# Performance work log

Measured on AMD Instinct MI355X. Metric: run time of the kernel, lower is better.

The kernel has to match this reference:

```python
import jax, jax.numpy as jnp
import numpy as np

ROI_SIZES = (3, 7, 11)
IMAGE_SIZE = 960.0


def setup_inputs() -> dict:
    key = jax.random.key(0)
    ks = jax.random.split(key, 12)
    B, C, H, W = 1, 64, 120, 120
    N = 4096
    feature_maps = jax.random.normal(ks[0], (B, C, H, W), jnp.float32)
    cx = jax.random.uniform(ks[1], (N,), jnp.float32, 100.0, 860.0)
    cy = jax.random.uniform(ks[2], (N,), jnp.float32, 100.0, 860.0)
    bw = jax.random.uniform(ks[3], (N,), jnp.float32, 20.0, 240.0)
    bh = jax.random.uniform(ks[4], (N,), jnp.float32, 20.0, 240.0)
    boxes = jnp.stack([cx - bw / 2, cy - bh / 2, cx + bw / 2, cy + bh / 2], axis=1)
    s = 0.05
    w1 = jax.random.normal(ks[5], (64, 128), jnp.float32) * s
    b1 = jnp.zeros((128,), jnp.float32)
    w2 = jax.random.normal(ks[6], (128, 64), jnp.float32) * s
    b2 = jnp.zeros((64,), jnp.float32)
    p1 = jax.random.normal(ks[7], (256, 128), jnp.float32) * s
    pb1 = jnp.zeros((128,), jnp.float32)
    p2 = jax.random.normal(ks[8], (128, 64), jnp.float32) * s
    pb2 = jnp.zeros((64,), jnp.float32)
    return dict(feature_maps=feature_maps, boxes=boxes, w1=w1, b1=b1, w2=w2, b2=b2,
                p1=p1, pb1=pb1, p2=p2, pb2=pb2)


def _roi_pool(fm0, boxes_norm, r):
    """affine_grid + bilinear grid_sample (align_corners=False, zeros pad) + global avg pool.
    fm0: [C,H,W], boxes_norm: [N,4] in [-1,1]. Returns [N,C]."""
    C, H, W = fm0.shape
    x1, y1, x2, y2 = boxes_norm[:, 0], boxes_norm[:, 1], boxes_norm[:, 2], boxes_norm[:, 3]
    cx = (x1 + x2) / 2
    cy = (y1 + y2) / 2
    bw = jnp.clip(x2 - x1, 1e-6, None)
    bh = jnp.clip(y2 - y1, 1e-6, None)
    # affine_grid base coords with align_corners=False: (2i+1)/r - 1
    lin = (2.0 * jnp.arange(r, dtype=jnp.float32) + 1.0) / r - 1.0
    gx = cx[:, None, None] + (bw / 2)[:, None, None] * lin[None, None, :]  # [N,r,r]
    gy = cy[:, None, None] + (bh / 2)[:, None, None] * lin[None, :, None]  # [N,r,r]
    # normalized -> pixel coords (align_corners=False)
    ix = ((gx + 1.0) * W - 1.0) / 2.0
    iy = ((gy + 1.0) * H - 1.0) / 2.0
    x0f = jnp.floor(ix)
    y0f = jnp.floor(iy)
    wx1 = ix - x0f
    wy1 = iy - y0f
    x0 = x0f.astype(jnp.int32)
    y0 = y0f.astype(jnp.int32)
    fm_flat = fm0.reshape(C, H * W)

    def corner(xi, yi, wt):
        valid = (xi >= 0) & (xi < W) & (yi >= 0) & (yi < H)
        xi_c = jnp.clip(xi, 0, W - 1)
        yi_c = jnp.clip(yi, 0, H - 1)
        idx = yi_c * W + xi_c  # [N,r,r]
        vals = jnp.take(fm_flat, idx.reshape(-1), axis=1).reshape(C, *idx.shape)  # [C,N,r,r]
        return vals * (wt * valid.astype(wt.dtype))[None]

    out = (corner(x0, y0, (1 - wx1) * (1 - wy1))
           + corner(x0 + 1, y0, wx1 * (1 - wy1))
           + corner(x0, y0 + 1, (1 - wx1) * wy1)
           + corner(x0 + 1, y0 + 1, wx1 * wy1))
    return out.mean(axis=(2, 3)).T  # [N,C]


def _shared_head(x, w1, b1, w2, b2):
    h = jax.nn.relu(x @ w1 + b1)
    return jax.nn.relu(h @ w2 + b2)


def reference(feature_maps, boxes, w1, b1, w2, b2, p1, pb1, p2, pb2):
    B, C, H, W = feature_maps.shape
    N = boxes.shape[0]
    boxes_norm = boxes / IMAGE_SIZE * 2.0 - 1.0
    fm0 = feature_maps[0]
    feats = []
    for r in ROI_SIZES:
        pooled = _roi_pool(fm0, boxes_norm, r)  # [N,C]
        feats.append(_shared_head(pooled, w1, b1, w2, b2))
    # global context: avg-pool full map, expand to N
    g = feature_maps.mean(axis=(2, 3))  # [B,C], B=1
    g = jnp.broadcast_to(g, (N, C))
    feats.append(_shared_head(g, w1, b1, w2, b2))
    concat = jnp.concatenate(feats, axis=1)  # [N, 4*64]
    h = jax.nn.relu(concat @ p1 + pb1)
    return jax.nn.relu(h @ p2 + pb2)
```

## Files before the change

kernel.cpp:

```cpp
#include <hip/hip_runtime.h>
#include <hip/hip_bf16.h>


#define HW 120
#define NPIX (HW * HW)

__global__ __launch_bounds__(256) void k_transpose_mean(
    const float* __restrict__ fm, float* __restrict__ fm_t,
    float* __restrict__ partial)
{
    __shared__ float tile[64][65];
    __shared__ float pr[4][64];
    const int t  = threadIdx.x;
    const int tx = t & 63;
    const int ty = t >> 6;
    const int pix0 = blockIdx.x * 64;

    #pragma unroll
    for (int k = 0; k < 16; ++k) {
        const int c = k * 4 + ty;
        tile[c][tx] = fm[c * NPIX + pix0 + tx];
    }
    __syncthreads();
    #pragma unroll
    for (int k = 0; k < 16; ++k) {
        const int p = k * 4 + ty;
        fm_t[(pix0 + p) * 64 + tx] = tile[tx][p];
    }
    float s = 0.f;
    #pragma unroll
    for (int k = 0; k < 16; ++k) s += tile[tx][ty * 16 + k];
    pr[ty][tx] = s;
    __syncthreads();
    if (t < 64)
        partial[blockIdx.x * 64 + t] = pr[0][t] + pr[1][t] + pr[2][t] + pr[3][t];
}

__global__ __launch_bounds__(256) void k_ghead(
    const float* __restrict__ partial,
    const float* __restrict__ w1, const float* __restrict__ b1,
    const float* __restrict__ w2, const float* __restrict__ b2,
    const float* __restrict__ p1, const float* __restrict__ pb1,
    float* __restrict__ f1pre)
{
    __shared__ float pr[4][64];
    __shared__ float g[64];
    __shared__ float h[128];
    __shared__ float gh[64];
    const int t = threadIdx.x;
    const int c = t & 63, q = t >> 6;
    float s = 0.f;
    for (int b = q; b < 225; b += 4) s += partial[b * 64 + c];
    pr[q][c] = s;
    __syncthreads();
    if (t < 64) g[t] = (pr[0][t] + pr[1][t] + pr[2][t] + pr[3][t]) * (1.f / 14400.f);
    __syncthreads();
    if (t < 128) {
        float a = b1[t];
        #pragma unroll 8
        for (int cc = 0; cc < 64; ++cc) a = fmaf(g[cc], w1[cc * 128 + t], a);
        h[t] = fmaxf(a, 0.f);
    }
    __syncthreads();
    if (t < 64) {
        float a = b2[t];
        #pragma unroll 8
        for (int k = 0; k < 128; ++k) a = fmaf(h[k], w2[k * 64 + t], a);
        gh[t] = fmaxf(a, 0.f);
    }
    __syncthreads();
    if (t < 128) {
        float a = pb1[t];
        #pragma unroll 8
        for (int j = 0; j < 64; ++j) a = fmaf(gh[j], p1[(192 + j) * 128 + t], a);
        f1pre[t] = a;
    }
}

template <int R>
__device__ __forceinline__ float4 gather_seg(
    const char* __restrict__ fb, int pg,
    float cx, float cy, float bw2, float bh2)
{
    constexpr float invR = 1.f / (float)R;
    constexpr float s2   = invR * invR;
    float ax = 0.f, ay = 0.f, az = 0.f, aw = 0.f;
    #pragma unroll 2
    for (int lp = pg; lp < R * R; lp += 4) {
        const int i = lp / R;
        const int j = lp - i * R;
        const float liny = (float)(2 * i + 1) * invR - 1.f;
        const float linx = (float)(2 * j + 1) * invR - 1.f;
        const float gy = cy + bh2 * liny;
        const float gx = cx + bw2 * linx;
        const float iy = ((gy + 1.f) * 120.f - 1.f) * 0.5f;
        const float ix = ((gx + 1.f) * 120.f - 1.f) * 0.5f;
        const float y0f = floorf(iy), x0f = floorf(ix);
        const float wy = iy - y0f,  wx = ix - x0f;
        const int y0 = (int)y0f, x0 = (int)x0f;
        const float vy0 = (y0 >= 0 && y0 < HW)      ? 1.f : 0.f;
        const float vy1 = (y0 >= -1 && y0 < HW - 1) ? 1.f : 0.f;
        const float vx0 = (x0 >= 0 && x0 < HW)      ? 1.f : 0.f;
        const float vx1 = (x0 >= -1 && x0 < HW - 1) ? 1.f : 0.f;
        const int x0c = min(max(x0, 0), HW - 1);
        const int x1c = min(max(x0 + 1, 0), HW - 1);
        const int y0c = min(max(y0, 0), HW - 1);
        const int y1c = min(max(y0 + 1, 0), HW - 1);
        const int o00 = (y0c * HW + x0c) * 256;
        const int o01 = (y0c * HW + x1c) * 256;
        const int o10 = (y1c * HW + x0c) * 256;
        const int o11 = (y1c * HW + x1c) * 256;
        const float w00 = (1.f - wx) * (1.f - wy) * s2 * (vy0 * vx0);
        const float w01 = wx * (1.f - wy) * s2 * (vy0 * vx1);
        const float w10 = (1.f - wx) * wy * s2 * (vy1 * vx0);
        const float w11 = wx * wy * s2 * (vy1 * vx1);
        const float4 v0 = *(const float4*)(fb + o00);
        const float4 v1 = *(const float4*)(fb + o01);
        const float4 v2 = *(const float4*)(fb + o10);
        const float4 v3 = *(const float4*)(fb + o11);
        ax = fmaf(w00, v0.x, ax); ay = fmaf(w00, v0.y, ay);
        az = fmaf(w00, v0.z, az); aw = fmaf(w00, v0.w, aw);
        ax = fmaf(w01, v1.x, ax); ay = fmaf(w01, v1.y, ay);
        az = fmaf(w01, v1.z, az); aw = fmaf(w01, v1.w, aw);
        ax = fmaf(w10, v2.x, ax); ay = fmaf(w10, v2.y, ay);
        az = fmaf(w10, v2.z, az); aw = fmaf(w10, v2.w, aw);
        ax = fmaf(w11, v3.x, ax); ay = fmaf(w11, v3.y, ay);
        az = fmaf(w11, v3.z, az); aw = fmaf(w11, v3.w, aw);
    }
    ax += __shfl_xor(ax, 16, 64); ay += __shfl_xor(ay, 16, 64);
    az += __shfl_xor(az, 16, 64); aw += __shfl_xor(aw, 16, 64);
    ax += __shfl_xor(ax, 32, 64); ay += __shfl_xor(ay, 32, 64);
    az += __shfl_xor(az, 32, 64); aw += __shfl_xor(aw, 32, 64);
    return make_float4(ax, ay, az, aw);
}

__global__ __launch_bounds__(256, 8) void k_fused(
    const float* __restrict__ fm_t, const float* __restrict__ boxes,
    const float* __restrict__ w1, const float* __restrict__ b1,
    const float* __restrict__ w2, const float* __restrict__ b2,
    const float* __restrict__ p1, const float* __restrict__ f1pre,
    const float* __restrict__ p2, const float* __restrict__ pb2,
    float* __restrict__ out, int N)
{
    __shared__ __align__(16) float xbufS[4][192];
    __shared__ __align__(16) float hbufS[4][384];
    __shared__ __align__(16) float cbufS[4][192];
    __shared__ __align__(16) float fbufS[4][128];

    const int t    = threadIdx.x;
    const int lane = t & 63;
    const int wid  = t >> 6;
    const int n    = blockIdx.x * 4 + wid;
    if (n >= N) return;

    float* xbuf = xbufS[wid];
    float* hbuf = hbufS[wid];
    float* cbuf = cbufS[wid];
    float* fbuf = fbufS[wid];

    const float4 bx = reinterpret_cast<const float4*>(boxes)[n];
    const float x1 = bx.x / 960.f * 2.f - 1.f;
    const float y1 = bx.y / 960.f * 2.f - 1.f;
    const float x2 = bx.z / 960.f * 2.f - 1.f;
    const float y2 = bx.w / 960.f * 2.f - 1.f;
    const float cx  = (x1 + x2) * 0.5f;
    const float cy  = (y1 + y2) * 0.5f;
    const float bw2 = fmaxf(x2 - x1, 1e-6f) * 0.5f;
    const float bh2 = fmaxf(y2 - y1, 1e-6f) * 0.5f;

    const int qc = lane & 15;
    const int pg = lane >> 4;
    const char* fb = (const char*)fm_t + qc * 16;

    const float4 r0 = gather_seg<3>(fb, pg, cx, cy, bw2, bh2);
    const float4 r1 = gather_seg<7>(fb, pg, cx, cy, bw2, bh2);
    const float4 r2 = gather_seg<11>(fb, pg, cx, cy, bw2, bh2);
    if (pg == 0) {
        *(float4*)(xbuf +       4 * qc) = r0;
        *(float4*)(xbuf +  64 + 4 * qc) = r1;
        *(float4*)(xbuf + 128 + 4 * qc) = r2;
    }

    float h0l, h0h, h1l, h1h, h2l, h2h;
    {
        const float bl = b1[lane], bh = b1[64 + lane];
        h0l = h1l = h2l = bl; h0h = h1h = h2h = bh;
        #define L1STEP(XA0, XA1, XA2, CC) {                                \
            const float wlo = w1[(CC) * 128 + lane];                       \
            const float whi = w1[(CC) * 128 + 64 + lane];                  \
            h0l = fmaf(XA0, wlo, h0l); h0h = fmaf(XA0, whi, h0h);          \
            h1l = fmaf(XA1, wlo, h1l); h1h = fmaf(XA1, whi, h1h);          \
            h2l = fmaf(XA2, wlo, h2l); h2h = fmaf(XA2, whi, h2h); }
        #pragma unroll 4
        for (int k4 = 0; k4 < 16; ++k4) {
            const float4 xv0 = *(const float4*)(xbuf +       4 * k4);
            const float4 xv1 = *(const float4*)(xbuf +  64 + 4 * k4);
            const float4 xv2 = *(const float4*)(xbuf + 128 + 4 * k4);
            L1STEP(xv0.x, xv1.x, xv2.x, 4 * k4 + 0)
            L1STEP(xv0.y, xv1.y, xv2.y, 4 * k4 + 1)
            L1STEP(xv0.z, xv1.z, xv2.z, 4 * k4 + 2)
            L1STEP(xv0.w, xv1.w, xv2.w, 4 * k4 + 3)
        }
        #undef L1STEP
        h0l = fmaxf(h0l, 0.f); h0h = fmaxf(h0h, 0.f);
        h1l = fmaxf(h1l, 0.f); h1h = fmaxf(h1h, 0.f);
        h2l = fmaxf(h2l, 0.f); h2h = fmaxf(h2h, 0.f);
        hbuf[lane]       = h0l; hbuf[64 + lane]  = h0h;
        hbuf[128 + lane] = h1l; hbuf[192 + lane] = h1h;
        hbuf[256 + lane] = h2l; hbuf[320 + lane] = h2h;
    }

    {
        const float bb = b2[lane];
        float c0 = bb, c1 = bb, c2 = bb;
        #define L2STEP(HA0, HA1, HA2, CC) {                                \
            const float wa = w2[(CC) * 64 + lane];                         \
            c0 = fmaf(HA0, wa, c0);                                        \
            c1 = fmaf(HA1, wa, c1);                                        \
            c2 = fmaf(HA2, wa, c2); }
        #pragma unroll 4
        for (int k4 = 0; k4 < 32; ++k4) {
            const float4 hv0 = *(const float4*)(hbuf +       4 * k4);
            const float4 hv1 = *(const float4*)(hbuf + 128 + 4 * k4);
            const float4 hv2 = *(const float4*)(hbuf + 256 + 4 * k4);
            L2STEP(hv0.x, hv1.x, hv2.x, 4 * k4 + 0)
            L2STEP(hv0.y, hv1.y, hv2.y, 4 * k4 + 1)
            L2STEP(hv0.z, hv1.z, hv2.z, 4 * k4 + 2)
            L2STEP(hv0.w, hv1.w, hv2.w, 4 * k4 + 3)
        }
        #undef L2STEP
        cbuf[lane]       = fmaxf(c0, 0.f);
        cbuf[64 + lane]  = fmaxf(c1, 0.f);
        cbuf[128 + lane] = fmaxf(c2, 0.f);
    }

    {
        float flo = f1pre[lane], fhi = f1pre[64 + lane];
        #define L3STEP(CA, QQ) {                                           \
            const float wlo = p1[(QQ) * 128 + lane];                       \
            const float whi = p1[(QQ) * 128 + 64 + lane];                  \
            flo = fmaf(CA, wlo, flo); fhi = fmaf(CA, whi, fhi); }
        #pragma unroll 4
        for (int q4 = 0; q4 < 48; ++q4) {
            const float4 cv = *(const float4*)(cbuf + 4 * q4);
            L3STEP(cv.x, 4 * q4 + 0)
            L3STEP(cv.y, 4 * q4 + 1)
            L3STEP(cv.z, 4 * q4 + 2)
            L3STEP(cv.w, 4 * q4 + 3)
        }
        #undef L3STEP
        fbuf[lane]      = fmaxf(flo, 0.f);
        fbuf[64 + lane] = fmaxf(fhi, 0.f);
    }

    {
        float o = pb2[lane];
        #define L4STEP(FA, JJ) o = fmaf(FA, p2[(JJ) * 64 + lane], o);
        #pragma unroll 4
        for (int j4 = 0; j4 < 32; ++j4) {
            const float4 fv = *(const float4*)(fbuf + 4 * j4);
            L4STEP(fv.x, 4 * j4 + 0)
            L4STEP(fv.y, 4 * j4 + 1)
            L4STEP(fv.z, 4 * j4 + 2)
            L4STEP(fv.w, 4 * j4 + 3)
        }
        #undef L4STEP
        out[n * 64 + lane] = fmaxf(o, 0.f);
    }
}

extern "C" void kernel_launch(void* const* d_in, const int* in_sizes, int n_in,
                              void* d_out, int out_size, void* d_ws, size_t ws_size,
                              hipStream_t stream)
{
    const float* fm    = (const float*)d_in[0];
    const float* boxes = (const float*)d_in[1];
    const float* w1    = (const float*)d_in[2];
    const float* b1    = (const float*)d_in[3];
    const float* w2    = (const float*)d_in[4];
    const float* b2    = (const float*)d_in[5];
    const float* p1    = (const float*)d_in[6];
    const float* pb1   = (const float*)d_in[7];
    const float* p2    = (const float*)d_in[8];
    const float* pb2   = (const float*)d_in[9];
    float* out = (float*)d_out;

    const int N = in_sizes[1] / 4;

    float* ws      = (float*)d_ws;
    float* fm_t    = ws;
    float* partial = fm_t + 921600;
    float* f1pre   = partial + 14400;

    k_transpose_mean<<<NPIX / 64, 256, 0, stream>>>(fm, fm_t, partial);
    k_ghead<<<1, 256, 0, stream>>>(partial, w1, b1, w2, b2, p1, pb1, f1pre);
    k_fused<<<(N + 3) / 4, 256, 0, stream>>>(fm_t, boxes, w1, b1, w2, b2,
                                             p1, f1pre, p2, pb2, out, N);
}
```

Measured before the change: 157.2 us.

## Split each ROI gather across two waves and share MLP work block-wide

The fused kernel goes from 256 to 512 threads per block. Each box's bilinear gather is now split over two waves, and the partial sums are reduced through shared memory. The MLP layers are redistributed so that all 512 threads cooperate across the block's 4 boxes, with __syncthreads between stages instead of one wave per box doing everything. This aims to raise parallelism and cut per-wave serial work, at the cost of block-wide barriers, more shared memory and a reduction step.

Measured after the change: 157.0 us. No clear change (-0.1%).

```diff
diff --git a/kernel.cpp b/kernel.cpp
--- a/kernel.cpp
+++ b/kernel.cpp
@@ -78,15 +78,15 @@
 }
 
 template <int R>
-__device__ __forceinline__ float4 gather_seg(
-    const char* __restrict__ fb, int pg,
+__device__ __forceinline__ float4 gather8(
+    const char* __restrict__ fb, int g8,
     float cx, float cy, float bw2, float bh2)
 {
     constexpr float invR = 1.f / (float)R;
     constexpr float s2   = invR * invR;
     float ax = 0.f, ay = 0.f, az = 0.f, aw = 0.f;
     #pragma unroll 2
-    for (int lp = pg; lp < R * R; lp += 4) {
+    for (int lp = g8; lp < R * R; lp += 8) {
         const int i = lp / R;
         const int j = lp - i * R;
         const float liny = (float)(2 * i + 1) * invR - 1.f;
@@ -134,7 +134,7 @@
     return make_float4(ax, ay, az, aw);
 }
 
-__global__ __launch_bounds__(256, 8) void k_fused(
+__global__ __launch_bounds__(512, 8) void k_fused(
     const float* __restrict__ fm_t, const float* __restrict__ boxes,
     const float* __restrict__ w1, const float* __restrict__ b1,
     const float* __restrict__ w2, const float* __restrict__ b2,
@@ -142,130 +142,166 @@
     const float* __restrict__ p2, const float* __restrict__ pb2,
     float* __restrict__ out, int N)
 {
-    __shared__ __align__(16) float xbufS[4][192];
-    __shared__ __align__(16) float hbufS[4][384];
-    __shared__ __align__(16) float cbufS[4][192];
-    __shared__ __align__(16) float fbufS[4][128];
+    __shared__ __align__(16) float xpart[4][2][192];
+    __shared__ __align__(16) float xbuf[4][192];
+    __shared__ __align__(16) float hbuf[4][384];
+    __shared__ __align__(16) float cbuf[4][192];
+    __shared__ __align__(16) float fbuf[4][128];
+    __shared__ __align__(16) float opart[2][4][64];
 
     const int t    = threadIdx.x;
     const int lane = t & 63;
-    const int wid  = t >> 6;
-    const int n    = blockIdx.x * 4 + wid;
-    if (n >= N) return;
-
-    float* xbuf = xbufS[wid];
-    float* hbuf = hbufS[wid];
-    float* cbuf = cbufS[wid];
-    float* fbuf = fbufS[wid];
-
-    const float4 bx = reinterpret_cast<const float4*>(boxes)[n];
-    const float x1 = bx.x / 960.f * 2.f - 1.f;
-    const float y1 = bx.y / 960.f * 2.f - 1.f;
-    const float x2 = bx.z / 960.f * 2.f - 1.f;
-    const float y2 = bx.w / 960.f * 2.f - 1.f;
-    const float cx  = (x1 + x2) * 0.5f;
-    const float cy  = (y1 + y2) * 0.5f;
-    const float bw2 = fmaxf(x2 - x1, 1e-6f) * 0.5f;
-    const float bh2 = fmaxf(y2 - y1, 1e-6f) * 0.5f;
-
-    const int qc = lane & 15;
-    const int pg = lane >> 4;
-    const char* fb = (const char*)fm_t + qc * 16;
-
-    const float4 r0 = gather_seg<3>(fb, pg, cx, cy, bw2, bh2);
-    const float4 r1 = gather_seg<7>(fb, pg, cx, cy, bw2, bh2);
-    const float4 r2 = gather_seg<11>(fb, pg, cx, cy, bw2, bh2);
-    if (pg == 0) {
-        *(float4*)(xbuf +       4 * qc) = r0;
-        *(float4*)(xbuf +  64 + 4 * qc) = r1;
-        *(float4*)(xbuf + 128 + 4 * qc) = r2;
-    }
-
-    float h0l, h0h, h1l, h1h, h2l, h2h;
-    {
-        const float bl = b1[lane], bh = b1[64 + lane];
-        h0l = h1l = h2l = bl; h0h = h1h = h2h = bh;
-        #define L1STEP(XA0, XA1, XA2, CC) {                                \
-            const float wlo = w1[(CC) * 128 + lane];                       \
-            const float whi = w1[(CC) * 128 + 64 + lane];                  \
-            h0l = fmaf(XA0, wlo, h0l); h0h = fmaf(XA0, whi, h0h);          \
-            h1l = fmaf(XA1, wlo, h1l); h1h = fmaf(XA1, whi, h1h);          \
-            h2l = fmaf(XA2, wlo, h2l); h2h = fmaf(XA2, whi, h2h); }
+    const int w    = t >> 6;
+    const int n0   = blockIdx.x * 4;
+
+    {
+        const int b  = w >> 1;
+        const int hf = w & 1;
+        const int qc = lane & 15;
+        const int pg = lane >> 4;
+        const int g8 = hf * 4 + pg;
+        const int n  = n0 + b;
+
+        if (n < N) {
+            const float4 bx = reinterpret_cast<const float4*>(boxes)[n];
+            const float x1 = bx.x / 960.f * 2.f - 1.f;
+            const float y1 = bx.y / 960.f * 2.f - 1.f;
+            const float x2 = bx.z / 960.f * 2.f - 1.f;
+            const float y2 = bx.w / 960.f * 2.f - 1.f;
+            const float cx  = (x1 + x2) * 0.5f;
+            const float cy  = (y1 + y2) * 0.5f;
+            const float bw2 = fmaxf(x2 - x1, 1e-6f) * 0.5f;
+            const float bh2 = fmaxf(y2 - y1, 1e-6f) * 0.5f;
+            const char* fb = (const char*)fm_t + qc * 16;
+
+            const float4 r0 = gather8<3>(fb, g8, cx, cy, bw2, bh2);
+            if (pg == 0) *(float4*)(&xpart[b][hf][4 * qc]) = r0;
+            const float4 r1 = gather8<7>(fb, g8, cx, cy, bw2, bh2);
+            if (pg == 0) *(float4*)(&xpart[b][hf][64 + 4 * qc]) = r1;
+            const float4 r2 = gather8<11>(fb, g8, cx, cy, bw2, bh2);
+            if (pg == 0) *(float4*)(&xpart[b][hf][128 + 4 * qc]) = r2;
+        } else if (pg == 0) {
+            const float4 z = make_float4(0.f, 0.f, 0.f, 0.f);
+            *(float4*)(&xpart[b][hf][4 * qc]) = z;
+            *(float4*)(&xpart[b][hf][64 + 4 * qc]) = z;
+            *(float4*)(&xpart[b][hf][128 + 4 * qc]) = z;
+        }
+    }
+    __syncthreads();
+
+    {
+        int i = t;
+        { const int b = i / 192, r = i - b * 192;
+          xbuf[b][r] = xpart[b][0][r] + xpart[b][1][r]; }
+        if (t < 256) {
+            i = 512 + t;
+            const int b = i / 192, r = i - b * 192;
+            xbuf[b][r] = xpart[b][0][r] + xpart[b][1][r];
+        }
+    }
+    __syncthreads();
+
+    {
+        const int k  = t & 127;
+        const int wp = t >> 7;
+        int b0, s0, b1_, s1_, b2_, s2_;
+        { const int G = wp;      b0 = G / 3;  s0 = G - 3 * b0; }
+        { const int G = 4 + wp;  b1_ = G / 3; s1_ = G - 3 * b1_; }
+        { const int G = 8 + wp;  b2_ = G / 3; s2_ = G - 3 * b2_; }
+        const float* xb0 = xbuf[b0] + s0 * 64;
+        const float* xb1 = xbuf[b1_] + s1_ * 64;
+        const float* xb2 = xbuf[b2_] + s2_ * 64;
+        const float bias = b1[k];
+        float a0 = bias, a1 = bias, a2 = bias;
         #pragma unroll 4
-        for (int k4 = 0; k4 < 16; ++k4) {
-            const float4 xv0 = *(const float4*)(xbuf +       4 * k4);
-            const float4 xv1 = *(const float4*)(xbuf +  64 + 4 * k4);
-            const float4 xv2 = *(const float4*)(xbuf + 128 + 4 * k4);
-            L1STEP(xv0.x, xv1.x, xv2.x, 4 * k4 + 0)
-            L1STEP(xv0.y, xv1.y, xv2.y, 4 * k4 + 1)
-            L1STEP(xv0.z, xv1.z, xv2.z, 4 * k4 + 2)
-            L1STEP(xv0.w, xv1.w, xv2.w, 4 * k4 + 3)
-        }
-        #undef L1STEP
-        h0l = fmaxf(h0l, 0.f); h0h = fmaxf(h0h, 0.f);
-        h1l = fmaxf(h1l, 0.f); h1h = fmaxf(h1h, 0.f);
-        h2l = fmaxf(h2l, 0.f); h2h = fmaxf(h2h, 0.f);
-        hbuf[lane]       = h0l; hbuf[64 + lane]  = h0h;
-        hbuf[128 + lane] = h1l; hbuf[192 + lane] = h1h;
-        hbuf[256 + lane] = h2l; hbuf[320 + lane] = h2h;
-    }
-
-    {
-        const float bb = b2[lane];
-        float c0 = bb, c1 = bb, c2 = bb;
-        #define L2STEP(HA0, HA1, HA2, CC) {                                \
-            const float wa = w2[(CC) * 64 + lane];                         \
-            c0 = fmaf(HA0, wa, c0);                                        \
-            c1 = fmaf(HA1, wa, c1);                                        \
-            c2 = fmaf(HA2, wa, c2); }
+        for (int c4 = 0; c4 < 16; ++c4) {
+            const float4 xv0 = *(const float4*)(xb0 + 4 * c4);
+            const float4 xv1 = *(const float4*)(xb1 + 4 * c4);
+            const float4 xv2 = *(const float4*)(xb2 + 4 * c4);
+            #define W1LD(CI) w1[(4 * c4 + CI) * 128 + k]
+            { const float wv = W1LD(0);
+              a0 = fmaf(xv0.x, wv, a0); a1 = fmaf(xv1.x, wv, a1); a2 = fmaf(xv2.x, wv, a2); }
+            { const float wv = W1LD(1);
+              a0 = fmaf(xv0.y, wv, a0); a1 = fmaf(xv1.y, wv, a1); a2 = fmaf(xv2.y, wv, a2); }
+            { const float wv = W1LD(2);
+              a0 = fmaf(xv0.z, wv, a0); a1 = fmaf(xv1.z, wv, a1); a2 = fmaf(xv2.z, wv, a2); }
+            { const float wv = W1LD(3);
+              a0 = fmaf(xv0.w, wv, a0); a1 = fmaf(xv1.w, wv, a1); a2 = fmaf(xv2.w, wv, a2); }
+            #undef W1LD
+        }
+        hbuf[b0][s0 * 128 + k]  = fmaxf(a0, 0.f);
+        hbuf[b1_][s1_ * 128 + k] = fmaxf(a1, 0.f);
+        hbuf[b2_][s2_ * 128 + k] = fmaxf(a2, 0.f);
+    }
+    __syncthreads();
+
+    {
+        const int co = lane;
+        const int G0 = w;
+        const int b0 = G0 / 3, s0 = G0 - 3 * b0;
+        const float* hb0 = hbuf[b0] + s0 * 128;
+        const bool two = (w < 4);
+        const int G1 = 8 + w;
+        const int b1_ = two ? (G1 / 3) : 0, s1_ = two ? (G1 - 3 * (G1 / 3)) : 0;
+        const float* hb1 = hbuf[b1_] + s1_ * 128;
+        const float bias = b2[co];
+        float a0 = bias, a1 = bias;
         #pragma unroll 4
-        for (int k4 = 0; k4 < 32; ++k4) {
-            const float4 hv0 = *(const float4*)(hbuf +       4 * k4);
-            const float4 hv1 = *(const float4*)(hbuf + 128 + 4 * k4);
-            const float4 hv2 = *(const float4*)(hbuf + 256 + 4 * k4);
-            L2STEP(hv0.x, hv1.x, hv2.x, 4 * k4 + 0)
-            L2STEP(hv0.y, hv1.y, hv2.y, 4 * k4 + 1)
-            L2STEP(hv0.z, hv1.z, hv2.z, 4 * k4 + 2)
-            L2STEP(hv0.w, hv1.w, hv2.w, 4 * k4 + 3)
-        }
-        #undef L2STEP
-        cbuf[lane]       = fmaxf(c0, 0.f);
-        cbuf[64 + lane]  = fmaxf(c1, 0.f);
-        cbuf[128 + lane] = fmaxf(c2, 0.f);
-    }
-
-    {
-        float flo = f1pre[lane], fhi = f1pre[64 + lane];
-        #define L3STEP(CA, QQ) {                                           \
-            const float wlo = p1[(QQ) * 128 + lane];                       \
-            const float whi = p1[(QQ) * 128 + 64 + lane];                  \
-            flo = fmaf(CA, wlo, flo); fhi = fmaf(CA, whi, fhi); }
+        for (int c4 = 0; c4 < 32; ++c4) {
+            const float4 hv0 = *(const float4*)(hb0 + 4 * c4);
+            const float4 hv1 = *(const float4*)(hb1 + 4 * c4);
+            #define W2LD(CI) w2[(4 * c4 + CI) * 64 + co]
+            { const float wv = W2LD(0); a0 = fmaf(hv0.x, wv, a0); a1 = fmaf(hv1.x, wv, a1); }
+            { const float wv = W2LD(1); a0 = fmaf(hv0.y, wv, a0); a1 = fmaf(hv1.y, wv, a1); }
+            { const float wv = W2LD(2); a0 = fmaf(hv0.z, wv, a0); a1 = fmaf(hv1.z, wv, a1); }
+            { const float wv = W2LD(3); a0 = fmaf(hv0.w, wv, a0); a1 = fmaf(hv1.w, wv, a1); }
+            #undef W2LD
+        }
+        cbuf[b0][s0 * 64 + co] = fmaxf(a0, 0.f);
+        if (two) cbuf[b1_][s1_ * 64 + co] = fmaxf(a1, 0.f);
+    }
+    __syncthreads();
+
+    {
+        const int k = t & 127;
+        const int b = t >> 7;
+        const float* cb = cbuf[b];
+        float a = f1pre[k];
         #pragma unroll 4
         for (int q4 = 0; q4 < 48; ++q4) {
-            const float4 cv = *(const float4*)(cbuf + 4 * q4);
-            L3STEP(cv.x, 4 * q4 + 0)
-            L3STEP(cv.y, 4 * q4 + 1)
-            L3STEP(cv.z, 4 * q4 + 2)
-            L3STEP(cv.w, 4 * q4 + 3)
-        }
-        #undef L3STEP
-        fbuf[lane]      = fmaxf(flo, 0.f);
-        fbuf[64 + lane] = fmaxf(fhi, 0.f);
-    }
-
-    {
-        float o = pb2[lane];
-        #define L4STEP(FA, JJ) o = fmaf(FA, p2[(JJ) * 64 + lane], o);
+            const float4 cv = *(const float4*)(cb + 4 * q4);
+            a = fmaf(cv.x, p1[(4 * q4 + 0) * 128 + k], a);
+            a = fmaf(cv.y, p1[(4 * q4 + 1) * 128 + k], a);
+            a = fmaf(cv.z, p1[(4 * q4 + 2) * 128 + k], a);
+            a = fmaf(cv.w, p1[(4 * q4 + 3) * 128 + k], a);
+        }
+        fbuf[b][k] = fmaxf(a, 0.f);
+    }
+    __syncthreads();
+
+    {
+        const int kh = t >> 8;
+        const int b  = (t >> 6) & 3;
+        const int co = lane;
+        const float* fbp = fbuf[b] + kh * 64;
+        float a = kh ? 0.f : pb2[co];
         #pragma unroll 4
-        for (int j4 = 0; j4 < 32; ++j4) {
-            const float4 fv = *(const float4*)(fbuf + 4 * j4);
-            L4STEP(fv.x, 4 * j4 + 0)
-            L4STEP(fv.y, 4 * j4 + 1)
-            L4STEP(fv.z, 4 * j4 + 2)
-            L4STEP(fv.w, 4 * j4 + 3)
-        }
-        #undef L4STEP
-        out[n * 64 + lane] = fmaxf(o, 0.f);
+        for (int j4 = 0; j4 < 16; ++j4) {
+            const float4 fv = *(const float4*)(fbp + 4 * j4);
+            a = fmaf(fv.x, p2[(kh * 64 + 4 * j4 + 0) * 64 + co], a);
+            a = fmaf(fv.y, p2[(kh * 64 + 4 * j4 + 1) * 64 + co], a);
+            a = fmaf(fv.z, p2[(kh * 64 + 4 * j4 + 2) * 64 + co], a);
+            a = fmaf(fv.w, p2[(kh * 64 + 4 * j4 + 3) * 64 + co], a);
+        }
+        opart[kh][b][co] = a;
+    }
+    __syncthreads();
+    if (t < 256) {
+        const int b  = t >> 6;
+        const int co = lane;
+        const int n  = n0 + b;
+        if (n < N)
+            out[n * 64 + co] = fmaxf(opart[0][b][co] + opart[1][b][co], 0.f);
     }
 }
 
@@ -294,6 +330,6 @@
 
     k_transpose_mean<<<NPIX / 64, 256, 0, stream>>>(fm, fm_t, partial);
     k_ghead<<<1, 256, 0, stream>>>(partial, w1, b1, w2, b2, p1, pb1, f1pre);
-    k_fused<<<(N + 3) / 4, 256, 0, stream>>>(fm_t, boxes, w1, b1, w2, b2,
+    k_fused<<<(N + 3) / 4, 512, 0, stream>>>(fm_t, boxes, w1, b1, w2, b2,
                                              p1, f1pre, p2, pb2, out, N);
 }
```
